# Optimization experiments

Measured on AMD Instinct MI355X. Metric: run time of the kernel, lower is better.

## Reference

```python
import jax, jax.numpy as jnp
import numpy as np

N = 30000   # vertices
E = 4000    # hyperedges
NNZ = 960000
D = 256
ALPHA = 0.1
BETA = 0.8


def setup_inputs() -> dict:
    key = jax.random.key(0)
    k1, k2, k3, k4, k5, k6 = jax.random.split(key, 6)
    X = jax.random.normal(k1, (N, D), dtype=jnp.float32)
    X0 = jax.random.normal(k2, (N, D), dtype=jnp.float32)
    H = jax.random.uniform(k3, (N, E), dtype=jnp.float32)
    vertex = jax.random.randint(k4, (NNZ,), 0, N, dtype=jnp.int64)
    edges = jax.random.randint(k5, (NNZ,), 0, E, dtype=jnp.int64)
    # Linear(in_features=256, out_features=256, bias=False) weight, torch layout [out, in]
    W = jax.random.normal(k6, (D, D), dtype=jnp.float32) * (1.0 / np.sqrt(D))
    return {"X": X, "X0": X0, "H": H, "W": W, "vertex": vertex, "edges": edges}


def reference(X, X0, H, W, vertex, edges):
    # degree scalings from dense incidence matrix
    degV = jnp.sum(H, axis=1) ** -0.5            # [N]
    degV = jnp.where(jnp.isinf(degV), 1.0, degV)[:, None]
    degE = (jnp.sum(H, axis=0) ** -0.5)[:, None]  # [E,1]

    Xve = X[vertex]                               # [nnz, d] gather
    # scatter-mean to edges
    sums = jax.ops.segment_sum(Xve, edges, num_segments=E)            # [E, d]
    cnt = jax.ops.segment_sum(jnp.ones((Xve.shape[0],), X.dtype), edges, num_segments=E)
    Xe = sums / jnp.maximum(cnt, 1.0)[:, None]
    Xe = Xe * degE

    Xev = Xe[edges]                               # [nnz, d] gather
    Xv = jax.ops.segment_sum(Xev, vertex, num_segments=X.shape[0])    # [N, d]
    Xv = Xv * degV

    Xi = (1.0 - ALPHA) * Xv + ALPHA * X0
    out = (1.0 - BETA) * Xi + BETA * (Xi @ W.T)
    return out
```

## Files before the change

### kernel.cpp

```cpp
#include <hip/hip_runtime.h>

#define D 256
#define ALPHA 0.1f
#define BETA 0.8f
#define CAPE 384
#define CAPV 96

typedef float v4f __attribute__((ext_vector_type(4)));
typedef float f32x4 __attribute__((ext_vector_type(4)));
typedef short bf16x8 __attribute__((ext_vector_type(8)));

__device__ __forceinline__ void add4(float4& a, const float4& b) {
    a.x += b.x; a.y += b.y; a.z += b.z; a.w += b.w;
}

__device__ __forceinline__ unsigned short f2bf(float f) {
    unsigned int u = __float_as_uint(f);
    u += 0x7FFFu + ((u >> 16) & 1u);
    return (unsigned short)(u >> 16);
}
__device__ __forceinline__ float bf2f(unsigned short h) {
    return __uint_as_float((unsigned int)h << 16);
}
__device__ __forceinline__ void addbf4(float4& a, const ushort4& t) {
    a.x += bf2f(t.x); a.y += bf2f(t.y); a.z += bf2f(t.z); a.w += bf2f(t.w);
}

__global__ __launch_bounds__(256) void k_init(const float* __restrict__ W,
                                              unsigned short* __restrict__ Wtb,
                                              float* __restrict__ colsum,
                                              int* __restrict__ cnt_e,
                                              int* __restrict__ cnt_v,
                                              const float* __restrict__ X,
                                              unsigned short* __restrict__ Xb,
                                              int n, int e, int total4) {
    int idx = blockIdx.x * 256 + threadIdx.x;
    if (idx < total4) {
        float4 x = reinterpret_cast<const float4*>(X)[idx];
        ushort4 b;
        b.x = f2bf(x.x); b.y = f2bf(x.y); b.z = f2bf(x.z); b.w = f2bf(x.w);
        reinterpret_cast<ushort4*>(Xb)[idx] = b;
    }
    if (idx < D * D) {
        int o = idx >> 8, i = idx & 255;
        Wtb[idx] = f2bf(BETA * W[idx] + ((i == o) ? (1.0f - BETA) : 0.0f));
    }
    if (idx < e) { colsum[idx] = 0.f; cnt_e[idx] = 0; }
    if (idx < n) cnt_v[idx] = 0;
}

__global__ __launch_bounds__(256) void k_build(const float* __restrict__ H,
                                               float* __restrict__ rowsum,
                                               float* __restrict__ colsum,
                                               const int* __restrict__ vertex,
                                               const int* __restrict__ edges,
                                               int* __restrict__ cnt_e,
                                               int* __restrict__ cnt_v,
                                               int* __restrict__ list_e,
                                               int* __restrict__ list_v,
                                               int n, int e, int nnz) {
    const int tid = threadIdx.x;
    const int b   = blockIdx.x;

    if ((b & 1) == 0) {
        const int rid  = b >> 1;
        const int wave = tid >> 6, lane = tid & 63;
        const int ec4  = e >> 2;
        __shared__ float4 sl[4][1000];

        float4 cp[16];
        #pragma unroll
        for (int k = 0; k < 16; ++k) cp[k] = make_float4(0.f, 0.f, 0.f, 0.f);

        const int rbase = rid * 32 + wave * 8;
        for (int i = 0; i < 8; ++i) {
            int row = rbase + i;
            float rs = 0.f;
            if (row < n) {
                const v4f* Hr = reinterpret_cast<const v4f*>(H + (size_t)row * e);
                float4 v[16];
                #pragma unroll
                for (int k = 0; k < 16; ++k) {
                    int s = lane + 64 * k;
                    if (s < ec4) {
                        v4f t = __builtin_nontemporal_load(Hr + s);
                        v[k] = make_float4(t.x, t.y, t.z, t.w);
                    } else {
                        v[k] = make_float4(0.f, 0.f, 0.f, 0.f);
                    }
                }
                #pragma unroll
                for (int k = 0; k < 16; ++k) {
                    rs += (v[k].x + v[k].y) + (v[k].z + v[k].w);
                    add4(cp[k], v[k]);
                }
            }
            #pragma unroll
            for (int s = 32; s > 0; s >>= 1) rs += __shfl_down(rs, s, 64);
            if (lane == 0 && row < n) rowsum[row] = rs;
        }

        #pragma unroll
        for (int k = 0; k < 16; ++k) {
            int s = lane + 64 * k;
            if (s < ec4) sl[wave][s] = cp[k];
        }
        __syncthreads();

        for (int c4 = tid; c4 < ec4; c4 += 256) {
            float4 s = sl[0][c4];
            add4(s, sl[1][c4]); add4(s, sl[2][c4]); add4(s, sl[3][c4]);
            atomicAdd(&colsum[4 * c4 + 0], s.x);
            atomicAdd(&colsum[4 * c4 + 1], s.y);
            atomicAdd(&colsum[4 * c4 + 2], s.z);
            atomicAdd(&colsum[4 * c4 + 3], s.w);
        }
    } else {
        const int fid = b >> 1;
        int base4 = ((fid * 256) + tid) * 4;
        if (base4 + 3 < nnz) {
            int4 ee = reinterpret_cast<const int4*>(edges)[base4 >> 2];
            int4 vv = reinterpret_cast<const int4*>(vertex)[base4 >> 2];
            int p0 = atomicAdd(&cnt_e[ee.x], 1);
            int p1 = atomicAdd(&cnt_e[ee.y], 1);
            int p2 = atomicAdd(&cnt_e[ee.z], 1);
            int p3 = atomicAdd(&cnt_e[ee.w], 1);
            int q0 = atomicAdd(&cnt_v[vv.x], 1);
            int q1 = atomicAdd(&cnt_v[vv.y], 1);
            int q2 = atomicAdd(&cnt_v[vv.z], 1);
            int q3 = atomicAdd(&cnt_v[vv.w], 1);
            if (p0 < CAPE) list_e[(size_t)ee.x * CAPE + p0] = vv.x;
            if (p1 < CAPE) list_e[(size_t)ee.y * CAPE + p1] = vv.y;
            if (p2 < CAPE) list_e[(size_t)ee.z * CAPE + p2] = vv.z;
            if (p3 < CAPE) list_e[(size_t)ee.w * CAPE + p3] = vv.w;
            if (q0 < CAPV) list_v[(size_t)vv.x * CAPV + q0] = ee.x;
            if (q1 < CAPV) list_v[(size_t)vv.y * CAPV + q1] = ee.y;
            if (q2 < CAPV) list_v[(size_t)vv.z * CAPV + q2] = ee.z;
            if (q3 < CAPV) list_v[(size_t)vv.w * CAPV + q3] = ee.w;
        } else {
            for (int i = base4; i < nnz; ++i) {
                int ee = edges[i], v = vertex[i];
                int p = atomicAdd(&cnt_e[ee], 1);
                if (p < CAPE) list_e[(size_t)ee * CAPE + p] = v;
                int q = atomicAdd(&cnt_v[v], 1);
                if (q < CAPV) list_v[(size_t)v * CAPV + q] = ee;
            }
        }
    }
}

__global__ __launch_bounds__(256) void k_edge_agg(const unsigned short* __restrict__ Xb,
                                                  const int* __restrict__ list_e,
                                                  const int* __restrict__ cnt_e,
                                                  const float* __restrict__ colsum,
                                                  unsigned short* __restrict__ Xeb, int e) {
    const int eid  = blockIdx.x * 4 + (threadIdx.x >> 6);
    const int lane = threadIdx.x & 63;
    if (eid >= e) return;
    const int cnt  = cnt_e[eid];
    const int m    = cnt < CAPE ? cnt : CAPE;
    const int j0   = eid * CAPE;

    float4 a[8];
    #pragma unroll
    for (int k = 0; k < 8; ++k) a[k] = make_float4(0.f, 0.f, 0.f, 0.f);

    int j = 0;
    for (; j + 7 < m; j += 8) {
        #pragma unroll
        for (int k = 0; k < 8; ++k) {
            int v = list_e[j0 + j + k];
            ushort4 t = reinterpret_cast<const ushort4*>(Xb + (size_t)v * D)[lane];
            addbf4(a[k], t);
        }
    }
    for (; j < m; ++j) {
        int v = list_e[j0 + j];
        ushort4 t = reinterpret_cast<const ushort4*>(Xb + (size_t)v * D)[lane];
        addbf4(a[0], t);
    }
    #pragma unroll
    for (int k = 1; k < 8; ++k) add4(a[0], a[k]);

    float scale = rsqrtf(colsum[eid]) / (float)(cnt > 0 ? cnt : 1);
    ushort4 o;
    o.x = f2bf(a[0].x * scale); o.y = f2bf(a[0].y * scale);
    o.z = f2bf(a[0].z * scale); o.w = f2bf(a[0].w * scale);
    reinterpret_cast<ushort4*>(Xeb + (size_t)eid * D)[lane] = o;
}

__global__ __launch_bounds__(256) void k_vertex_agg(const unsigned short* __restrict__ Xeb,
                                                    const int* __restrict__ list_v,
                                                    const int* __restrict__ cnt_v,
                                                    const float* __restrict__ rowsum,
                                                    const float* __restrict__ X0,
                                                    unsigned short* __restrict__ Xib, int n) {
    const int v    = blockIdx.x * 4 + (threadIdx.x >> 6);
    const int lane = threadIdx.x & 63;
    if (v >= n) return;
    const int cnt  = cnt_v[v];
    const int m    = cnt < CAPV ? cnt : CAPV;
    const int j0   = v * CAPV;

    float4 a[4];
    #pragma unroll
    for (int k = 0; k < 4; ++k) a[k] = make_float4(0.f, 0.f, 0.f, 0.f);

    int j = 0;
    for (; j + 3 < m; j += 4) {
        #pragma unroll
        for (int k = 0; k < 4; ++k) {
            int e = list_v[j0 + j + k];
            ushort4 t = reinterpret_cast<const ushort4*>(Xeb + (size_t)e * D)[lane];
            addbf4(a[k], t);
        }
    }
    for (; j < m; ++j) {
        int e = list_v[j0 + j];
        ushort4 t = reinterpret_cast<const ushort4*>(Xeb + (size_t)e * D)[lane];
        addbf4(a[0], t);
    }
    add4(a[0], a[1]); add4(a[2], a[3]); add4(a[0], a[2]);

    float rs = rowsum[v];
    float degV = (rs > 0.f) ? rsqrtf(rs) : 1.0f;
    float scale = (1.0f - ALPHA) * degV;
    float4 x0 = reinterpret_cast<const float4*>(X0 + (size_t)v * D)[lane];
    ushort4 o;
    o.x = f2bf(scale * a[0].x + ALPHA * x0.x);
    o.y = f2bf(scale * a[0].y + ALPHA * x0.y);
    o.z = f2bf(scale * a[0].z + ALPHA * x0.z);
    o.w = f2bf(scale * a[0].w + ALPHA * x0.w);
    reinterpret_cast<ushort4*>(Xib + (size_t)v * D)[lane] = o;
}

__global__ __launch_bounds__(256) void k_gemm_mfma(const unsigned short* __restrict__ A,
                                                   const unsigned short* __restrict__ B,
                                                   float* __restrict__ C, int n) {
    const int wave = threadIdx.x >> 6;
    const int lane = threadIdx.x & 63;
    const int m0 = (blockIdx.x * 4 + wave) * 16;
    if (m0 >= n) return;
    const int arow = lane & 15;
    const int kgrp = lane >> 4;

    f32x4 acc[16];
    #pragma unroll
    for (int c = 0; c < 16; ++c) acc[c] = (f32x4){0.f, 0.f, 0.f, 0.f};

    const unsigned short* aptr = A + (size_t)(m0 + arow) * D + kgrp * 8;
    const unsigned short* bptr = B + (size_t)arow * D + kgrp * 8;

    for (int kk = 0; kk < D; kk += 32) {
        bf16x8 afrag = *reinterpret_cast<const bf16x8*>(aptr + kk);
        #pragma unroll
        for (int c = 0; c < 16; ++c) {
            bf16x8 bfrag = *reinterpret_cast<const bf16x8*>(bptr + (size_t)c * 16 * D + kk);
            acc[c] = __builtin_amdgcn_mfma_f32_16x16x32_bf16(afrag, bfrag, acc[c], 0, 0, 0);
        }
    }

    #pragma unroll
    for (int c = 0; c < 16; ++c) {
        #pragma unroll
        for (int r = 0; r < 4; ++r) {
            int row = m0 + kgrp * 4 + r;
            C[(size_t)row * D + c * 16 + arow] = acc[c][r];
        }
    }
}

extern "C" void kernel_launch(void* const* d_in, const int* in_sizes, int n_in,
                              void* d_out, int out_size, void* d_ws, size_t ws_size,
                              hipStream_t stream) {
    const float* X      = (const float*)d_in[0];
    const float* X0     = (const float*)d_in[1];
    const float* H      = (const float*)d_in[2];
    const float* W      = (const float*)d_in[3];
    const int*   vertex = (const int*)d_in[4];
    const int*   edges  = (const int*)d_in[5];
    float* out = (float*)d_out;

    const int n   = in_sizes[0] / D;
    const int e   = in_sizes[2] / n;
    const int nnz = in_sizes[4];

    char* base = (char*)d_ws;
    size_t off = 0;
    auto carve = [&](size_t bytes) {
        size_t o = off;
        off += (bytes + 255) & ~(size_t)255;
        return o;
    };
    unsigned short* Xib    = (unsigned short*)(base + carve((size_t)n * D * 2));
    unsigned short* Xb     = (unsigned short*)(base + carve((size_t)n * D * 2));
    unsigned short* Xeb    = (unsigned short*)(base + carve((size_t)e * D * 2));
    unsigned short* Wtb    = (unsigned short*)(base + carve((size_t)D * D * 2));
    float*          rowsum = (float*)(base + carve((size_t)n * 4));
    float*          colsum = (float*)(base + carve((size_t)e * 4));
    int*            cnt_e  = (int*)(base + carve((size_t)e * 4));
    int*            cnt_v  = (int*)(base + carve((size_t)n * 4));
    int*            list_e = (int*)(base + carve((size_t)e * CAPE * 4));
    int*            list_v = (int*)(base + carve((size_t)n * CAPV * 4));
    (void)ws_size; (void)n_in; (void)out_size;

    const int nRowBlk  = (n + 31) / 32;
    const int nFillBlk = (nnz / 4 + 255) / 256;
    const int total4   = n * D / 4;
    const int nInitBlk = (total4 + 255) / 256;

    k_init<<<dim3(nInitBlk), dim3(256), 0, stream>>>(W, Wtb, colsum, cnt_e, cnt_v,
                                                     X, Xb, n, e, total4);
    k_build<<<dim3(nRowBlk + nFillBlk), dim3(256), 0, stream>>>(
        H, rowsum, colsum, vertex, edges, cnt_e, cnt_v, list_e, list_v, n, e, nnz);
    k_edge_agg<<<dim3((e + 3) / 4), dim3(256), 0, stream>>>(Xb, list_e, cnt_e, colsum, Xeb, e);
    k_vertex_agg<<<dim3((n + 3) / 4), dim3(256), 0, stream>>>(Xeb, list_v, cnt_v, rowsum, X0, Xib, n);
    k_gemm_mfma<<<dim3((n / 16 + 3) / 4), dim3(256), 0, stream>>>(Xib, Wtb, out, n);
}
```

Before: 403.2 us.

## Prepack weight into MFMA fragment layout and split GEMM columns across waves

The combined weight matrix is now stored pre-swizzled in MFMA B-fragment order, so each lane's B load is a contiguous 16-byte read with the 64 lanes of a wave reading adjacent addresses. The GEMM now assigns two waves to each 16-row tile, each wave covering half the output columns, with all A fragments preloaded into registers. This doubles the grid size and cuts per-wave accumulators, aiming for more parallelism and better-coalesced B loads. The cost is that every A tile is read twice and there is more packing work in the init kernel. The GEMM is only the last of several stages, so overall impact is limited.

```diff
diff --git a/kernel.cpp b/kernel.cpp
--- a/kernel.cpp
+++ b/kernel.cpp
@@ -27,7 +27,7 @@
 }
 
 __global__ __launch_bounds__(256) void k_init(const float* __restrict__ W,
-                                              unsigned short* __restrict__ Wtb,
+                                              unsigned short* __restrict__ Bp,
                                               float* __restrict__ colsum,
                                               int* __restrict__ cnt_e,
                                               int* __restrict__ cnt_v,
@@ -41,9 +41,20 @@
         b.x = f2bf(x.x); b.y = f2bf(x.y); b.z = f2bf(x.z); b.w = f2bf(x.w);
         reinterpret_cast<ushort4*>(Xb)[idx] = b;
     }
-    if (idx < D * D) {
-        int o = idx >> 8, i = idx & 255;
-        Wtb[idx] = f2bf(BETA * W[idx] + ((i == o) ? (1.0f - BETA) : 0.0f));
+    if (idx < 8192) {
+        int c    = idx >> 9;
+        int kk   = (idx >> 6) & 7;
+        int lane = idx & 63;
+        int col   = c * 16 + (lane & 15);
+        int kbase = kk * 32 + (lane >> 4) * 8;
+        unsigned short tmp[8];
+        #pragma unroll
+        for (int j = 0; j < 8; ++j) {
+            int k = kbase + j;
+            float w = BETA * W[(size_t)col * D + k] + ((col == k) ? (1.0f - BETA) : 0.0f);
+            tmp[j] = f2bf(w);
+        }
+        reinterpret_cast<uint4*>(Bp)[idx] = *reinterpret_cast<const uint4*>(tmp);
     }
     if (idx < e) { colsum[idx] = 0.f; cnt_e[idx] = 0; }
     if (idx < n) cnt_v[idx] = 0;
@@ -235,37 +246,43 @@
 }
 
 __global__ __launch_bounds__(256) void k_gemm_mfma(const unsigned short* __restrict__ A,
-                                                   const unsigned short* __restrict__ B,
+                                                   const unsigned short* __restrict__ Bp,
                                                    float* __restrict__ C, int n) {
-    const int wave = threadIdx.x >> 6;
+    const int wv   = threadIdx.x >> 6;
     const int lane = threadIdx.x & 63;
-    const int m0 = (blockIdx.x * 4 + wave) * 16;
+    const int m0   = (blockIdx.x * 2 + (wv >> 1)) * 16;
+    const int nh   = wv & 1;
     if (m0 >= n) return;
     const int arow = lane & 15;
     const int kgrp = lane >> 4;
 
-    f32x4 acc[16];
-    #pragma unroll
-    for (int c = 0; c < 16; ++c) acc[c] = (f32x4){0.f, 0.f, 0.f, 0.f};
-
+    bf16x8 af[8];
     const unsigned short* aptr = A + (size_t)(m0 + arow) * D + kgrp * 8;
-    const unsigned short* bptr = B + (size_t)arow * D + kgrp * 8;
-
-    for (int kk = 0; kk < D; kk += 32) {
-        bf16x8 afrag = *reinterpret_cast<const bf16x8*>(aptr + kk);
-        #pragma unroll
-        for (int c = 0; c < 16; ++c) {
-            bf16x8 bfrag = *reinterpret_cast<const bf16x8*>(bptr + (size_t)c * 16 * D + kk);
-            acc[c] = __builtin_amdgcn_mfma_f32_16x16x32_bf16(afrag, bfrag, acc[c], 0, 0, 0);
-        }
-    }
-
-    #pragma unroll
-    for (int c = 0; c < 16; ++c) {
+    #pragma unroll
+    for (int k = 0; k < 8; ++k)
+        af[k] = *reinterpret_cast<const bf16x8*>(aptr + k * 32);
+
+    f32x4 acc[8];
+    #pragma unroll
+    for (int c = 0; c < 8; ++c) acc[c] = (f32x4){0.f, 0.f, 0.f, 0.f};
+
+    const bf16x8* bp = reinterpret_cast<const bf16x8*>(Bp) + ((size_t)nh * 8 * 8) * 64 + lane;
+    #pragma unroll
+    for (int c = 0; c < 8; ++c) {
+        #pragma unroll
+        for (int k = 0; k < 8; ++k) {
+            bf16x8 bf = bp[(size_t)(c * 8 + k) * 64];
+            acc[c] = __builtin_amdgcn_mfma_f32_16x16x32_bf16(af[k], bf, acc[c], 0, 0, 0);
+        }
+    }
+
+    const int cbase = nh * 8;
+    #pragma unroll
+    for (int c = 0; c < 8; ++c) {
         #pragma unroll
         for (int r = 0; r < 4; ++r) {
             int row = m0 + kgrp * 4 + r;
-            C[(size_t)row * D + c * 16 + arow] = acc[c][r];
+            C[(size_t)row * D + (cbase + c) * 16 + arow] = acc[c][r];
         }
     }
 }
@@ -295,7 +312,7 @@
     unsigned short* Xib    = (unsigned short*)(base + carve((size_t)n * D * 2));
     unsigned short* Xb     = (unsigned short*)(base + carve((size_t)n * D * 2));
     unsigned short* Xeb    = (unsigned short*)(base + carve((size_t)e * D * 2));
-    unsigned short* Wtb    = (unsigned short*)(base + carve((size_t)D * D * 2));
+    unsigned short* Bp     = (unsigned short*)(base + carve((size_t)D * D * 2));
     float*          rowsum = (float*)(base + carve((size_t)n * 4));
     float*          colsum = (float*)(base + carve((size_t)e * 4));
     int*            cnt_e  = (int*)(base + carve((size_t)e * 4));
@@ -309,11 +326,11 @@
     const int total4   = n * D / 4;
     const int nInitBlk = (total4 + 255) / 256;
 
-    k_init<<<dim3(nInitBlk), dim3(256), 0, stream>>>(W, Wtb, colsum, cnt_e, cnt_v,
+    k_init<<<dim3(nInitBlk), dim3(256), 0, stream>>>(W, Bp, colsum, cnt_e, cnt_v,
                                                      X, Xb, n, e, total4);
     k_build<<<dim3(nRowBlk + nFillBlk), dim3(256), 0, stream>>>(
         H, rowsum, colsum, vertex, edges, cnt_e, cnt_v, list_e, list_v, n, e, nnz);
     k_edge_agg<<<dim3((e + 3) / 4), dim3(256), 0, stream>>>(Xb, list_e, cnt_e, colsum, Xeb, e);
     k_vertex_agg<<<dim3((n + 3) / 4), dim3(256), 0, stream>>>(Xeb, list_v, cnt_v, rowsum, X0, Xib, n);
-    k_gemm_mfma<<<dim3((n / 16 + 3) / 4), dim3(256), 0, stream>>>(Xib, Wtb, out, n);
-}
+    k_gemm_mfma<<<dim3((n / 16 + 1) / 2), dim3(256), 0, stream>>>(Xib, Bp, out, n);
+}
```

After: 386.4 us. 4.2% less time.
